# Performance work log

Measured on AMD Instinct MI355X. Metric: run time of the kernel, lower is better.

Reference implementation:

```python
import math
import jax, jax.numpy as jnp
import numpy as np

B, S, HID, NH = 4, 1024, 768, 12
D = HID // NH
R_ACT = 0.5
R_ATTN = 0.5


def act_prune_mask(a, ratio):
    # per-sample kth-smallest magnitude threshold (torch.kthvalue on flatten(1))
    n = int(np.prod(a.shape[1:]))
    k = int(np.clip(n * ratio, 1, n))
    mag = jnp.abs(a)
    thr = jnp.sort(mag.reshape(a.shape[0], -1), axis=1)[:, k - 1]
    thr = thr.reshape((a.shape[0],) + (1,) * (a.ndim - 1))
    return mag >= thr


def setup_inputs() -> dict:
    key = jax.random.key(0)
    ks = jax.random.split(key, 5)
    inp = {
        "hidden_states": jax.random.normal(ks[0], (B, S, HID), dtype=jnp.float32),
        "Wq": jax.random.normal(ks[1], (HID, HID), dtype=jnp.float32) * 0.02,
        "bq": jnp.zeros((HID,), dtype=jnp.float32),
        "Wk": jax.random.normal(ks[2], (HID, HID), dtype=jnp.float32) * 0.02,
        "bk": jnp.zeros((HID,), dtype=jnp.float32),
        "Wv": jax.random.normal(ks[3], (HID, HID), dtype=jnp.float32) * 0.02,
        "bv": jnp.zeros((HID,), dtype=jnp.float32),
        "Wo": jax.random.normal(ks[4], (HID, HID), dtype=jnp.float32) * 0.02,
        "bo": jnp.zeros((HID,), dtype=jnp.float32),
    }
    return inp


def reference(hidden_states, Wq, bq, Wk, bk, Wv, bv, Wo, bo):
    b, s, hid = hidden_states.shape

    # prune mask on input activations (saved for backward in the original; forward math unchanged)
    mask_h = act_prune_mask(hidden_states, R_ACT)
    _hs_prune = jnp.where(mask_h, hidden_states, 0.0)

    q = jnp.matmul(hidden_states, Wq.T) + bq
    k = jnp.matmul(hidden_states, Wk.T) + bk
    v = jnp.matmul(hidden_states, Wv.T) + bv

    def split_heads(x):
        return x.reshape(b, s, NH, D).transpose(0, 2, 1, 3)  # [B,H,S,D]

    q4, k4, v4 = split_heads(q), split_heads(k), split_heads(v)

    mask_q = act_prune_mask(q4, R_ACT)
    mask_k = act_prune_mask(k4, R_ACT)
    _qp = jnp.where(mask_q, q4, 0.0)
    _kp = jnp.where(mask_k, k4, 0.0)

    scores = jnp.einsum("bhqd,bhkd->bhqk", q4, k4) / math.sqrt(D)
    probs = jax.nn.softmax(scores, axis=-1)

    mask_p = act_prune_mask(probs, R_ATTN)
    _pp = jnp.where(mask_p, probs, 0.0)
    mask_v = act_prune_mask(v4, R_ACT)
    _vp = jnp.where(mask_v, v4, 0.0)

    ctx = jnp.einsum("bhqk,bhkd->bhqd", probs, v4)
    ctx = ctx.transpose(0, 2, 1, 3).reshape(b, s, hid)

    mask_c = act_prune_mask(ctx, R_ACT)
    _cp = jnp.where(mask_c, ctx, 0.0)

    out = jnp.matmul(ctx, Wo.T) + bo  # proj_dropout rate = 0.0 (identity)
    return (out, probs)  # vis=True -> weights = attention_probs
```

## Files before the change

### kernel.cpp

```cpp
#include <hip/hip_runtime.h>
#include <hip/hip_bf16.h>

typedef __attribute__((ext_vector_type(4))) float f32x4;
typedef __attribute__((ext_vector_type(8))) short bf16x8;
typedef __attribute__((ext_vector_type(4))) int i32x4;

#define SEQ 1024
#define HIDV 768
#define NH 12
#define HD 64
#define QBLK 64

static __device__ __forceinline__ unsigned short f2b(float f) {
  unsigned u = __builtin_bit_cast(unsigned, f);
  u = (u + 0x7fffu + ((u >> 16) & 1u)) >> 16;
  return (unsigned short)u;
}

static __device__ __forceinline__ void gl16(const unsigned short* g, unsigned short* l) {
  __builtin_amdgcn_global_load_lds(
      (const __attribute__((address_space(1))) unsigned int*)g,
      (__attribute__((address_space(3))) unsigned int*)l, 16, 0, 0);
}

static __device__ __forceinline__ void bar_lgkm() {
  asm volatile("s_waitcnt lgkmcnt(0)" ::: "memory");
  __builtin_amdgcn_sched_barrier(0);
  __builtin_amdgcn_s_barrier();
  __builtin_amdgcn_sched_barrier(0);
}
static __device__ __forceinline__ void bar_only() {
  __builtin_amdgcn_sched_barrier(0);
  __builtin_amdgcn_s_barrier();
  __builtin_amdgcn_sched_barrier(0);
}

__global__ __launch_bounds__(256) void convert_all(
    const float* __restrict__ X, const float* __restrict__ Wq,
    const float* __restrict__ Wk, const float* __restrict__ Wv,
    const float* __restrict__ Wo, unsigned short* __restrict__ dst) {
  long i = (long)blockIdx.x * 256 + threadIdx.x;
  const long N4 = (3145728L + 4 * 589824L) / 4;
  if (i >= N4) return;
  long e = i * 4;
  const float* src; long off;
  if (e < 3145728L)      { src = X;  off = e; }
  else if (e < 3735552L) { src = Wq; off = e - 3145728L; }
  else if (e < 4325376L) { src = Wk; off = e - 3735552L; }
  else if (e < 4915200L) { src = Wv; off = e - 4325376L; }
  else                   { src = Wo; off = e - 4915200L; }
  const float4 v = *reinterpret_cast<const float4*>(src + off);
  ushort4 o;
  o.x = f2b(v.x); o.y = f2b(v.y); o.z = f2b(v.z); o.w = f2b(v.w);
  *reinterpret_cast<ushort4*>(dst + e) = o;
}

__global__ __launch_bounds__(256) void qkv_gemm(
    const unsigned short* __restrict__ Xb,
    const unsigned short* __restrict__ Wqb, const unsigned short* __restrict__ Wkb,
    const unsigned short* __restrict__ Wvb,
    const float* __restrict__ bq, const float* __restrict__ bk, const float* __restrict__ bv,
    unsigned short* __restrict__ Qh, unsigned short* __restrict__ Kh,
    unsigned short* __restrict__ VT) {
  __shared__ __align__(16) unsigned short la[2][128 * 32];
  __shared__ __align__(16) unsigned short lb[2][128 * 32];
  const int z = blockIdx.z;
  const unsigned short* Wb = (z == 0) ? Wqb : (z == 1) ? Wkb : Wvb;
  const float* bias = (z == 0) ? bq : (z == 1) ? bk : bv;
  const int m0 = blockIdx.x * 128, n0 = blockIdx.y * 128;
  const int tid = threadIdx.x;
  const int wave = tid >> 6, lane = tid & 63, g = lane >> 4, c = lane & 15;
  const int wr = (wave >> 1) * 64, wc = (wave & 1) * 64;

  const int sr = wave * 16 + (lane >> 2);
  const int scol = (lane & 3) * 8;
  const unsigned short* Ag = &Xb[(size_t)(m0 + sr) * HIDV + scol];
  const unsigned short* Bg = &Wb[(size_t)(n0 + sr) * HIDV + scol];

  gl16(Ag, &la[0][(wave * 16) * 32]);
  gl16(Ag + (size_t)64 * HIDV, &la[0][(64 + wave * 16) * 32]);
  gl16(Bg, &lb[0][(wave * 16) * 32]);
  gl16(Bg + (size_t)64 * HIDV, &lb[0][(64 + wave * 16) * 32]);
  __syncthreads();

  f32x4 acc[4][4] = {};
  for (int t = 0; t < 24; t++) {
    const int cur = t & 1;
    if (t < 23) {
      const int kt = (t + 1) * 32;
      gl16(Ag + kt, &la[cur ^ 1][(wave * 16) * 32]);
      gl16(Ag + (size_t)64 * HIDV + kt, &la[cur ^ 1][(64 + wave * 16) * 32]);
      gl16(Bg + kt, &lb[cur ^ 1][(wave * 16) * 32]);
      gl16(Bg + (size_t)64 * HIDV + kt, &lb[cur ^ 1][(64 + wave * 16) * 32]);
    }
    bf16x8 af[4], bfr[4];
#pragma unroll
    for (int m = 0; m < 4; m++)
      af[m] = *reinterpret_cast<bf16x8*>(&la[cur][(wr + m * 16 + c) * 32 + g * 8]);
#pragma unroll
    for (int n = 0; n < 4; n++)
      bfr[n] = *reinterpret_cast<bf16x8*>(&lb[cur][(wc + n * 16 + c) * 32 + g * 8]);
#pragma unroll
    for (int m = 0; m < 4; m++)
#pragma unroll
      for (int n = 0; n < 4; n++)
        acc[m][n] = __builtin_amdgcn_mfma_f32_16x16x32_bf16(af[m], bfr[n], acc[m][n], 0, 0, 0);
    __syncthreads();
  }
  float bv4[4];
#pragma unroll
  for (int n = 0; n < 4; n++) bv4[n] = bias[n0 + wc + n * 16 + c];
  if (z < 2) {
    unsigned short* dst = (z == 0) ? Qh : Kh;
#pragma unroll
    for (int m = 0; m < 4; m++) {
      int rb_ = m0 + wr + m * 16 + g * 4;
#pragma unroll
      for (int n = 0; n < 4; n++) {
        int col = n0 + wc + n * 16 + c;
        int h = col >> 6, d = col & 63;
#pragma unroll
        for (int r = 0; r < 4; r++) {
          int row = rb_ + r;
          int b = row >> 10, s = row & 1023;
          dst[((size_t)(b * NH + h) * SEQ + s) * HD + d] = f2b(acc[m][n][r] + bv4[n]);
        }
      }
    }
  } else {
#pragma unroll
    for (int m = 0; m < 4; m++) {
      int rb_ = m0 + wr + m * 16 + g * 4;
      int b = rb_ >> 10, s = rb_ & 1023;
#pragma unroll
      for (int n = 0; n < 4; n++) {
        int col = n0 + wc + n * 16 + c;
        int h = col >> 6, d = col & 63;
        ushort4 o;
        o.x = f2b(acc[m][n][0] + bv4[n]);
        o.y = f2b(acc[m][n][1] + bv4[n]);
        o.z = f2b(acc[m][n][2] + bv4[n]);
        o.w = f2b(acc[m][n][3] + bv4[n]);
        *reinterpret_cast<ushort4*>(&VT[((size_t)(b * NH + h) * HD + d) * SEQ + s]) = o;
      }
    }
  }
}

#define EXPC 0.18033688f
__global__ __launch_bounds__(256) void attn_fused(
    const unsigned short* __restrict__ Qh, const unsigned short* __restrict__ Kh,
    const unsigned short* __restrict__ VT,
    float* __restrict__ probs, unsigned short* __restrict__ CTX) {
  __shared__ __align__(16) unsigned short ldsk[2][64 * 72];
  __shared__ __align__(16) unsigned short ldsv[2][64 * 72];
  __shared__ __align__(16) unsigned short lp[64 * 72];
  const int lin = blockIdx.x;
  const int swz = (lin & 7) * 96 + (lin >> 3);
  const int bh = swz >> 4, rb = (swz & 15) * QBLK;
  const int b = bh / NH, h = bh - b * NH;
  const unsigned short* Qp = Qh + (size_t)bh * SEQ * HD;
  const unsigned short* Kp = Kh + (size_t)bh * SEQ * HD;
  const unsigned short* Vp = VT + (size_t)bh * HD * SEQ;
  float* P = probs + (size_t)bh * SEQ * SEQ;
  const int tid = threadIdx.x, wave = tid >> 6, lane = tid & 63, g = lane >> 4, c = lane & 15;
  const int wrow = wave * 16;
  const int str = tid >> 3;
  const int stc = (tid & 7) * 8;

  bf16x8 aq[2];
#pragma unroll
  for (int ks = 0; ks < 2; ks++)
    aq[ks] = *reinterpret_cast<const bf16x8*>(&Qp[(size_t)(rb + wrow + c) * HD + ks * 32 + g * 8]);

  i32x4 kr0, kr1, vr0, vr1;
  kr0 = *reinterpret_cast<const i32x4*>(&Kp[(size_t)str * HD + stc]);
  kr1 = *reinterpret_cast<const i32x4*>(&Kp[(size_t)(str + 32) * HD + stc]);
  *reinterpret_cast<i32x4*>(&ldsk[0][str * 72 + stc]) = kr0;
  *reinterpret_cast<i32x4*>(&ldsk[0][(str + 32) * 72 + stc]) = kr1;
  bar_lgkm();

  float lsum = 0.f;
  for (int ct = 0; ct < 16; ct++) {
    const int cur = ct & 1;
    if (ct < 15) {
      kr0 = *reinterpret_cast<const i32x4*>(&Kp[(size_t)((ct + 1) * 64 + str) * HD + stc]);
      kr1 = *reinterpret_cast<const i32x4*>(&Kp[(size_t)((ct + 1) * 64 + str + 32) * HD + stc]);
    }
    f32x4 sreg[4] = {};
#pragma unroll
    for (int ks = 0; ks < 2; ks++) {
      bf16x8 kf[4];
#pragma unroll
      for (int kb = 0; kb < 4; kb++)
        kf[kb] = *reinterpret_cast<bf16x8*>(&ldsk[cur][(kb * 16 + c) * 72 + ks * 32 + g * 8]);
#pragma unroll
      for (int kb = 0; kb < 4; kb++)
        sreg[kb] = __builtin_amdgcn_mfma_f32_16x16x32_bf16(kf[kb], aq[ks], sreg[kb], 0, 0, 0);
    }
#pragma unroll
    for (int kb = 0; kb < 4; kb++)
#pragma unroll
      for (int r = 0; r < 4; r++)
        lsum += __builtin_amdgcn_exp2f(sreg[kb][r] * EXPC);
    if (ct < 15) {
      *reinterpret_cast<i32x4*>(&ldsk[cur ^ 1][str * 72 + stc]) = kr0;
      *reinterpret_cast<i32x4*>(&ldsk[cur ^ 1][(str + 32) * 72 + stc]) = kr1;
      bar_lgkm();
    }
  }
  float s = lsum;
  s += __shfl_xor(s, 16);
  s += __shfl_xor(s, 32);
  const float linv = 1.f / s;

  kr0 = *reinterpret_cast<const i32x4*>(&Kp[(size_t)str * HD + stc]);
  kr1 = *reinterpret_cast<const i32x4*>(&Kp[(size_t)(str + 32) * HD + stc]);
  vr0 = *reinterpret_cast<const i32x4*>(&Vp[(size_t)str * SEQ + stc]);
  vr1 = *reinterpret_cast<const i32x4*>(&Vp[(size_t)(str + 32) * SEQ + stc]);
  *reinterpret_cast<i32x4*>(&ldsk[0][str * 72 + stc]) = kr0;
  *reinterpret_cast<i32x4*>(&ldsk[0][(str + 32) * 72 + stc]) = kr1;
  *reinterpret_cast<i32x4*>(&ldsv[0][str * 72 + stc]) = vr0;
  *reinterpret_cast<i32x4*>(&ldsv[0][(str + 32) * 72 + stc]) = vr1;
  bar_lgkm();

  f32x4 acc[4] = {};
  for (int ct = 0; ct < 16; ct++) {
    const int cur = ct & 1;
    if (ct < 15) {
      kr0 = *reinterpret_cast<const i32x4*>(&Kp[(size_t)((ct + 1) * 64 + str) * HD + stc]);
      kr1 = *reinterpret_cast<const i32x4*>(&Kp[(size_t)((ct + 1) * 64 + str + 32) * HD + stc]);
      vr0 = *reinterpret_cast<const i32x4*>(&Vp[(size_t)str * SEQ + (ct + 1) * 64 + stc]);
      vr1 = *reinterpret_cast<const i32x4*>(&Vp[(size_t)(str + 32) * SEQ + (ct + 1) * 64 + stc]);
    }
    f32x4 sreg[4] = {};
#pragma unroll
    for (int ks = 0; ks < 2; ks++) {
      bf16x8 kf[4];
#pragma unroll
      for (int kb = 0; kb < 4; kb++)
        kf[kb] = *reinterpret_cast<bf16x8*>(&ldsk[cur][(kb * 16 + c) * 72 + ks * 32 + g * 8]);
#pragma unroll
      for (int kb = 0; kb < 4; kb++)
        sreg[kb] = __builtin_amdgcn_mfma_f32_16x16x32_bf16(kf[kb], aq[ks], sreg[kb], 0, 0, 0);
    }
    {
      float* Prow = &P[(size_t)(rb + wrow + c) * SEQ + ct * 64];
#pragma unroll
      for (int kb = 0; kb < 4; kb++) {
        f32x4 p;
#pragma unroll
        for (int r = 0; r < 4; r++)
          p[r] = __builtin_amdgcn_exp2f(sreg[kb][r] * EXPC) * linv;
        *reinterpret_cast<f32x4*>(&Prow[kb * 16 + g * 4]) = p;
        uint2 pk;
        pk.x = (unsigned)f2b(p[0]) | ((unsigned)f2b(p[1]) << 16);
        pk.y = (unsigned)f2b(p[2]) | ((unsigned)f2b(p[3]) << 16);
        *reinterpret_cast<uint2*>(&lp[(wrow + c) * 72 + kb * 16 + g * 4]) = pk;
      }
    }
    if (ct < 15) {
      *reinterpret_cast<i32x4*>(&ldsk[cur ^ 1][str * 72 + stc]) = kr0;
      *reinterpret_cast<i32x4*>(&ldsk[cur ^ 1][(str + 32) * 72 + stc]) = kr1;
      *reinterpret_cast<i32x4*>(&ldsv[cur ^ 1][str * 72 + stc]) = vr0;
      *reinterpret_cast<i32x4*>(&ldsv[cur ^ 1][(str + 32) * 72 + stc]) = vr1;
    }
    bar_lgkm();
#pragma unroll
    for (int ks = 0; ks < 2; ks++) {
      bf16x8 pa, vf[4];
      pa = *reinterpret_cast<bf16x8*>(&lp[(wrow + c) * 72 + ks * 32 + g * 8]);
#pragma unroll
      for (int db = 0; db < 4; db++)
        vf[db] = *reinterpret_cast<bf16x8*>(&ldsv[cur][(db * 16 + c) * 72 + ks * 32 + g * 8]);
#pragma unroll
      for (int db = 0; db < 4; db++)
        acc[db] = __builtin_amdgcn_mfma_f32_16x16x32_bf16(pa, vf[db], acc[db], 0, 0, 0);
    }
    bar_only();
  }

#pragma unroll
  for (int db = 0; db < 4; db++)
#pragma unroll
    for (int r = 0; r < 4; r++)
      lp[(wrow + g * 4 + r) * 72 + db * 16 + c] = f2b(acc[db][r]);
  bar_lgkm();
  {
    const int q = tid >> 2, seg = (tid & 3) * 16;
    const unsigned short* src = &lp[q * 72 + seg];
    unsigned short* dst = &CTX[(size_t)(b * SEQ + rb + q) * HIDV + h * HD + seg];
    i32x4 t0 = *reinterpret_cast<const i32x4*>(&src[0]);
    i32x4 t1 = *reinterpret_cast<const i32x4*>(&src[8]);
    *reinterpret_cast<i32x4*>(&dst[0]) = t0;
    *reinterpret_cast<i32x4*>(&dst[8]) = t1;
  }
}

__global__ __launch_bounds__(256) void proj_gemm(
    const unsigned short* __restrict__ Ab, const unsigned short* __restrict__ Wb,
    const float* __restrict__ bias, float* __restrict__ out) {
  __shared__ __align__(16) unsigned short la[2][128 * 32];
  __shared__ __align__(16) unsigned short lb[2][128 * 32];
  const int m0 = blockIdx.x * 128, n0 = blockIdx.y * 128;
  const int tid = threadIdx.x;
  const int wave = tid >> 6, lane = tid & 63, g = lane >> 4, c = lane & 15;
  const int wr = (wave >> 1) * 64, wc = (wave & 1) * 64;
  const int sr = wave * 16 + (lane >> 2);
  const int scol = (lane & 3) * 8;
  const unsigned short* Ag = &Ab[(size_t)(m0 + sr) * HIDV + scol];
  const unsigned short* Bg = &Wb[(size_t)(n0 + sr) * HIDV + scol];

  gl16(Ag, &la[0][(wave * 16) * 32]);
  gl16(Ag + (size_t)64 * HIDV, &la[0][(64 + wave * 16) * 32]);
  gl16(Bg, &lb[0][(wave * 16) * 32]);
  gl16(Bg + (size_t)64 * HIDV, &lb[0][(64 + wave * 16) * 32]);
  __syncthreads();

  f32x4 acc[4][4] = {};
  for (int t = 0; t < 24; t++) {
    const int cur = t & 1;
    if (t < 23) {
      const int kt = (t + 1) * 32;
      gl16(Ag + kt, &la[cur ^ 1][(wave * 16) * 32]);
      gl16(Ag + (size_t)64 * HIDV + kt, &la[cur ^ 1][(64 + wave * 16) * 32]);
      gl16(Bg + kt, &lb[cur ^ 1][(wave * 16) * 32]);
      gl16(Bg + (size_t)64 * HIDV + kt, &lb[cur ^ 1][(64 + wave * 16) * 32]);
    }
    bf16x8 af[4], bfr[4];
#pragma unroll
    for (int m = 0; m < 4; m++)
      af[m] = *reinterpret_cast<bf16x8*>(&la[cur][(wr + m * 16 + c) * 32 + g * 8]);
#pragma unroll
    for (int n = 0; n < 4; n++)
      bfr[n] = *reinterpret_cast<bf16x8*>(&lb[cur][(wc + n * 16 + c) * 32 + g * 8]);
#pragma unroll
    for (int m = 0; m < 4; m++)
#pragma unroll
      for (int n = 0; n < 4; n++)
        acc[m][n] = __builtin_amdgcn_mfma_f32_16x16x32_bf16(af[m], bfr[n], acc[m][n], 0, 0, 0);
    __syncthreads();
  }
  float bv4[4];
#pragma unroll
  for (int n = 0; n < 4; n++) bv4[n] = bias[n0 + wc + n * 16 + c];
#pragma unroll
  for (int m = 0; m < 4; m++) {
    int rb_ = m0 + wr + m * 16 + g * 4;
#pragma unroll
    for (int n = 0; n < 4; n++) {
      int col = n0 + wc + n * 16 + c;
#pragma unroll
      for (int r = 0; r < 4; r++)
        out[(size_t)(rb_ + r) * HIDV + col] = acc[m][n][r] + bv4[n];
    }
  }
}

extern "C" void kernel_launch(void* const* d_in, const int* in_sizes, int n_in,
                              void* d_out, int out_size, void* d_ws, size_t ws_size,
                              hipStream_t stream) {
  const float* X  = (const float*)d_in[0];
  const float* Wq = (const float*)d_in[1];
  const float* bq = (const float*)d_in[2];
  const float* Wk = (const float*)d_in[3];
  const float* bk = (const float*)d_in[4];
  const float* Wv = (const float*)d_in[5];
  const float* bv = (const float*)d_in[6];
  const float* Wo = (const float*)d_in[7];
  const float* bo = (const float*)d_in[8];
  float* out = (float*)d_out;
  float* probs = out + 3145728;

  unsigned short* Xb  = (unsigned short*)d_ws;
  unsigned short* Wqb = Xb + 3145728;
  unsigned short* Wkb = Wqb + 589824;
  unsigned short* Wvb = Wkb + 589824;
  unsigned short* Wob = Wvb + 589824;
  unsigned short* Qh  = Wob + 589824;
  unsigned short* Kh  = Qh + 3145728;
  unsigned short* VT  = Kh + 3145728;
  unsigned short* CTX = VT + 3145728;

  convert_all<<<5376, 256, 0, stream>>>(X, Wq, Wk, Wv, Wo, Xb);
  qkv_gemm<<<dim3(32, 6, 3), 256, 0, stream>>>(Xb, Wqb, Wkb, Wvb, bq, bk, bv, Qh, Kh, VT);
  attn_fused<<<dim3(768), 256, 0, stream>>>(Qh, Kh, VT, probs, CTX);
  proj_gemm<<<dim3(32, 6), 256, 0, stream>>>(CTX, Wob, bo, out);
}
```

Baseline: 113.4 us.

## Triple-buffer GEMM loads, unroll attention loops by two, halve proj tile

The QKV and projection GEMMs move from double to triple-buffered global_load_lds staging with a prefetch distance of two, waiting with partial vmcnt counts instead of full syncthreads. The attention kernel's K/V register prefetch is unrolled by two with separate register sets, so loads for the next-next tile are issued before the current tile's compute. The projection GEMM uses 64-row M tiles to launch twice as many blocks. The aim is to hide global memory latency and raise occupancy, at the cost of more LDS and registers and tricky wait-count correctness.

```diff
diff --git a/kernel.cpp b/kernel.cpp
--- a/kernel.cpp
+++ b/kernel.cpp
@@ -34,6 +34,13 @@
   __builtin_amdgcn_s_barrier();
   __builtin_amdgcn_sched_barrier(0);
 }
+#define BAR_VM(N)                                                         \
+  do {                                                                    \
+    asm volatile("s_waitcnt vmcnt(" #N ") lgkmcnt(0)" ::: "memory");      \
+    __builtin_amdgcn_sched_barrier(0);                                    \
+    __builtin_amdgcn_s_barrier();                                         \
+    __builtin_amdgcn_sched_barrier(0);                                    \
+  } while (0)
 
 __global__ __launch_bounds__(256) void convert_all(
     const float* __restrict__ X, const float* __restrict__ Wq,
@@ -62,8 +69,8 @@
     const float* __restrict__ bq, const float* __restrict__ bk, const float* __restrict__ bv,
     unsigned short* __restrict__ Qh, unsigned short* __restrict__ Kh,
     unsigned short* __restrict__ VT) {
-  __shared__ __align__(16) unsigned short la[2][128 * 32];
-  __shared__ __align__(16) unsigned short lb[2][128 * 32];
+  __shared__ __align__(16) unsigned short la[3][128 * 32];
+  __shared__ __align__(16) unsigned short lb[3][128 * 32];
   const int z = blockIdx.z;
   const unsigned short* Wb = (z == 0) ? Wqb : (z == 1) ? Wkb : Wvb;
   const float* bias = (z == 0) ? bq : (z == 1) ? bk : bv;
@@ -77,22 +84,23 @@
   const unsigned short* Ag = &Xb[(size_t)(m0 + sr) * HIDV + scol];
   const unsigned short* Bg = &Wb[(size_t)(n0 + sr) * HIDV + scol];
 
-  gl16(Ag, &la[0][(wave * 16) * 32]);
-  gl16(Ag + (size_t)64 * HIDV, &la[0][(64 + wave * 16) * 32]);
-  gl16(Bg, &lb[0][(wave * 16) * 32]);
-  gl16(Bg + (size_t)64 * HIDV, &lb[0][(64 + wave * 16) * 32]);
-  __syncthreads();
+#define QKV_STAGE(buf, kt)                                                \
+  do {                                                                    \
+    gl16(Ag + (kt), &la[buf][(wave * 16) * 32]);                          \
+    gl16(Ag + (size_t)64 * HIDV + (kt), &la[buf][(64 + wave * 16) * 32]); \
+    gl16(Bg + (kt), &lb[buf][(wave * 16) * 32]);                          \
+    gl16(Bg + (size_t)64 * HIDV + (kt), &lb[buf][(64 + wave * 16) * 32]); \
+  } while (0)
+
+  QKV_STAGE(0, 0);
+  QKV_STAGE(1, 32);
+  BAR_VM(4);
 
   f32x4 acc[4][4] = {};
+#pragma unroll 3
   for (int t = 0; t < 24; t++) {
-    const int cur = t & 1;
-    if (t < 23) {
-      const int kt = (t + 1) * 32;
-      gl16(Ag + kt, &la[cur ^ 1][(wave * 16) * 32]);
-      gl16(Ag + (size_t)64 * HIDV + kt, &la[cur ^ 1][(64 + wave * 16) * 32]);
-      gl16(Bg + kt, &lb[cur ^ 1][(wave * 16) * 32]);
-      gl16(Bg + (size_t)64 * HIDV + kt, &lb[cur ^ 1][(64 + wave * 16) * 32]);
-    }
+    const int cur = t % 3;
+    if (t < 22) QKV_STAGE((t + 2) % 3, (t + 2) * 32);
     bf16x8 af[4], bfr[4];
 #pragma unroll
     for (int m = 0; m < 4; m++)
@@ -105,8 +113,10 @@
 #pragma unroll
       for (int n = 0; n < 4; n++)
         acc[m][n] = __builtin_amdgcn_mfma_f32_16x16x32_bf16(af[m], bfr[n], acc[m][n], 0, 0, 0);
-    __syncthreads();
-  }
+    if (t < 22)      BAR_VM(4);
+    else if (t < 23) BAR_VM(0);
+  }
+#undef QKV_STAGE
   float bv4[4];
 #pragma unroll
   for (int n = 0; n < 4; n++) bv4[n] = bias[n0 + wc + n * 16 + c];
@@ -173,112 +183,142 @@
   for (int ks = 0; ks < 2; ks++)
     aq[ks] = *reinterpret_cast<const bf16x8*>(&Qp[(size_t)(rb + wrow + c) * HD + ks * 32 + g * 8]);
 
-  i32x4 kr0, kr1, vr0, vr1;
-  kr0 = *reinterpret_cast<const i32x4*>(&Kp[(size_t)str * HD + stc]);
-  kr1 = *reinterpret_cast<const i32x4*>(&Kp[(size_t)(str + 32) * HD + stc]);
-  *reinterpret_cast<i32x4*>(&ldsk[0][str * 72 + stc]) = kr0;
-  *reinterpret_cast<i32x4*>(&ldsk[0][(str + 32) * 72 + stc]) = kr1;
+#define LDK(t, r0, r1)                                                               \
+  do {                                                                               \
+    r0 = *reinterpret_cast<const i32x4*>(&Kp[(size_t)((t)*64 + str) * HD + stc]);    \
+    r1 = *reinterpret_cast<const i32x4*>(&Kp[(size_t)((t)*64 + str + 32) * HD + stc]); \
+  } while (0)
+#define LDV(t, r0, r1)                                                               \
+  do {                                                                               \
+    r0 = *reinterpret_cast<const i32x4*>(&Vp[(size_t)str * SEQ + (t)*64 + stc]);     \
+    r1 = *reinterpret_cast<const i32x4*>(&Vp[(size_t)(str + 32) * SEQ + (t)*64 + stc]); \
+  } while (0)
+#define DSWK(buf, r0, r1)                                              \
+  do {                                                                 \
+    *reinterpret_cast<i32x4*>(&ldsk[buf][str * 72 + stc]) = r0;        \
+    *reinterpret_cast<i32x4*>(&ldsk[buf][(str + 32) * 72 + stc]) = r1; \
+  } while (0)
+#define DSWV(buf, r0, r1)                                              \
+  do {                                                                 \
+    *reinterpret_cast<i32x4*>(&ldsv[buf][str * 72 + stc]) = r0;        \
+    *reinterpret_cast<i32x4*>(&ldsv[buf][(str + 32) * 72 + stc]) = r1; \
+  } while (0)
+#define QKT_TILE(buf, sreg)                                                              \
+  do {                                                                                   \
+    _Pragma("unroll") for (int ks = 0; ks < 2; ks++) {                                   \
+      bf16x8 kf[4];                                                                      \
+      _Pragma("unroll") for (int kb = 0; kb < 4; kb++)                                   \
+          kf[kb] = *reinterpret_cast<bf16x8*>(&ldsk[buf][(kb * 16 + c) * 72 + ks * 32 + g * 8]); \
+      _Pragma("unroll") for (int kb = 0; kb < 4; kb++)                                   \
+          sreg[kb] = __builtin_amdgcn_mfma_f32_16x16x32_bf16(kf[kb], aq[ks], sreg[kb], 0, 0, 0); \
+    }                                                                                    \
+  } while (0)
+
+  i32x4 kA0, kA1, kB0, kB1;
+
+  float lsum = 0.f;
+  LDK(0, kA0, kA1);
+  LDK(1, kB0, kB1);
+  DSWK(0, kA0, kA1);
   bar_lgkm();
-
-  float lsum = 0.f;
-  for (int ct = 0; ct < 16; ct++) {
-    const int cur = ct & 1;
-    if (ct < 15) {
-      kr0 = *reinterpret_cast<const i32x4*>(&Kp[(size_t)((ct + 1) * 64 + str) * HD + stc]);
-      kr1 = *reinterpret_cast<const i32x4*>(&Kp[(size_t)((ct + 1) * 64 + str + 32) * HD + stc]);
-    }
-    f32x4 sreg[4] = {};
-#pragma unroll
-    for (int ks = 0; ks < 2; ks++) {
-      bf16x8 kf[4];
+#pragma unroll 1
+  for (int ct2 = 0; ct2 < 8; ct2++) {
+    const int ct = ct2 * 2;
+    if (ct2 < 7) LDK(ct + 2, kA0, kA1);
+    {
+      f32x4 sreg[4] = {};
+      QKT_TILE(0, sreg);
 #pragma unroll
       for (int kb = 0; kb < 4; kb++)
-        kf[kb] = *reinterpret_cast<bf16x8*>(&ldsk[cur][(kb * 16 + c) * 72 + ks * 32 + g * 8]);
+#pragma unroll
+        for (int r = 0; r < 4; r++) lsum += __builtin_amdgcn_exp2f(sreg[kb][r] * EXPC);
+    }
+    DSWK(1, kB0, kB1);
+    bar_lgkm();
+    if (ct2 < 7) LDK(ct + 3, kB0, kB1);
+    {
+      f32x4 sreg[4] = {};
+      QKT_TILE(1, sreg);
 #pragma unroll
       for (int kb = 0; kb < 4; kb++)
-        sreg[kb] = __builtin_amdgcn_mfma_f32_16x16x32_bf16(kf[kb], aq[ks], sreg[kb], 0, 0, 0);
-    }
-#pragma unroll
-    for (int kb = 0; kb < 4; kb++)
-#pragma unroll
-      for (int r = 0; r < 4; r++)
-        lsum += __builtin_amdgcn_exp2f(sreg[kb][r] * EXPC);
-    if (ct < 15) {
-      *reinterpret_cast<i32x4*>(&ldsk[cur ^ 1][str * 72 + stc]) = kr0;
-      *reinterpret_cast<i32x4*>(&ldsk[cur ^ 1][(str + 32) * 72 + stc]) = kr1;
-      bar_lgkm();
-    }
+#pragma unroll
+        for (int r = 0; r < 4; r++) lsum += __builtin_amdgcn_exp2f(sreg[kb][r] * EXPC);
+    }
+    if (ct2 < 7) DSWK(0, kA0, kA1);
+    bar_lgkm();
   }
   float s = lsum;
   s += __shfl_xor(s, 16);
   s += __shfl_xor(s, 32);
   const float linv = 1.f / s;
 
-  kr0 = *reinterpret_cast<const i32x4*>(&Kp[(size_t)str * HD + stc]);
-  kr1 = *reinterpret_cast<const i32x4*>(&Kp[(size_t)(str + 32) * HD + stc]);
-  vr0 = *reinterpret_cast<const i32x4*>(&Vp[(size_t)str * SEQ + stc]);
-  vr1 = *reinterpret_cast<const i32x4*>(&Vp[(size_t)(str + 32) * SEQ + stc]);
-  *reinterpret_cast<i32x4*>(&ldsk[0][str * 72 + stc]) = kr0;
-  *reinterpret_cast<i32x4*>(&ldsk[0][(str + 32) * 72 + stc]) = kr1;
-  *reinterpret_cast<i32x4*>(&ldsv[0][str * 72 + stc]) = vr0;
-  *reinterpret_cast<i32x4*>(&ldsv[0][(str + 32) * 72 + stc]) = vr1;
+#define PWRITE(ct, sreg)                                                      \
+  do {                                                                        \
+    float* Prow = &P[(size_t)(rb + wrow + c) * SEQ + (ct)*64];                \
+    _Pragma("unroll") for (int kb = 0; kb < 4; kb++) {                        \
+      f32x4 p;                                                                \
+      _Pragma("unroll") for (int r = 0; r < 4; r++)                           \
+          p[r] = __builtin_amdgcn_exp2f(sreg[kb][r] * EXPC) * linv;           \
+      *reinterpret_cast<f32x4*>(&Prow[kb * 16 + g * 4]) = p;                  \
+      uint2 pk;                                                               \
+      pk.x = (unsigned)f2b(p[0]) | ((unsigned)f2b(p[1]) << 16);               \
+      pk.y = (unsigned)f2b(p[2]) | ((unsigned)f2b(p[3]) << 16);               \
+      *reinterpret_cast<uint2*>(&lp[(wrow + c) * 72 + kb * 16 + g * 4]) = pk; \
+    }                                                                         \
+  } while (0)
+#define PV_TILE(buf)                                                                     \
+  do {                                                                                   \
+    _Pragma("unroll") for (int ks = 0; ks < 2; ks++) {                                   \
+      bf16x8 pa, vf[4];                                                                  \
+      pa = *reinterpret_cast<bf16x8*>(&lp[(wrow + c) * 72 + ks * 32 + g * 8]);           \
+      _Pragma("unroll") for (int db = 0; db < 4; db++)                                   \
+          vf[db] = *reinterpret_cast<bf16x8*>(&ldsv[buf][(db * 16 + c) * 72 + ks * 32 + g * 8]); \
+      _Pragma("unroll") for (int db = 0; db < 4; db++)                                   \
+          acc[db] = __builtin_amdgcn_mfma_f32_16x16x32_bf16(pa, vf[db], acc[db], 0, 0, 0); \
+    }                                                                                    \
+  } while (0)
+
+  i32x4 vA0, vA1, vB0, vB1;
+  f32x4 acc[4] = {};
+  LDK(0, kA0, kA1);
+  LDV(0, vA0, vA1);
+  LDK(1, kB0, kB1);
+  LDV(1, vB0, vB1);
+  DSWK(0, kA0, kA1);
+  DSWV(0, vA0, vA1);
   bar_lgkm();
-
-  f32x4 acc[4] = {};
-  for (int ct = 0; ct < 16; ct++) {
-    const int cur = ct & 1;
-    if (ct < 15) {
-      kr0 = *reinterpret_cast<const i32x4*>(&Kp[(size_t)((ct + 1) * 64 + str) * HD + stc]);
-      kr1 = *reinterpret_cast<const i32x4*>(&Kp[(size_t)((ct + 1) * 64 + str + 32) * HD + stc]);
-      vr0 = *reinterpret_cast<const i32x4*>(&Vp[(size_t)str * SEQ + (ct + 1) * 64 + stc]);
-      vr1 = *reinterpret_cast<const i32x4*>(&Vp[(size_t)(str + 32) * SEQ + (ct + 1) * 64 + stc]);
-    }
-    f32x4 sreg[4] = {};
-#pragma unroll
-    for (int ks = 0; ks < 2; ks++) {
-      bf16x8 kf[4];
-#pragma unroll
-      for (int kb = 0; kb < 4; kb++)
-        kf[kb] = *reinterpret_cast<bf16x8*>(&ldsk[cur][(kb * 16 + c) * 72 + ks * 32 + g * 8]);
-#pragma unroll
-      for (int kb = 0; kb < 4; kb++)
-        sreg[kb] = __builtin_amdgcn_mfma_f32_16x16x32_bf16(kf[kb], aq[ks], sreg[kb], 0, 0, 0);
-    }
+#pragma unroll 1
+  for (int ct2 = 0; ct2 < 8; ct2++) {
+    const int ct = ct2 * 2;
+    if (ct2 < 7) { LDK(ct + 2, kA0, kA1); LDV(ct + 2, vA0, vA1); }
     {
-      float* Prow = &P[(size_t)(rb + wrow + c) * SEQ + ct * 64];
-#pragma unroll
-      for (int kb = 0; kb < 4; kb++) {
-        f32x4 p;
-#pragma unroll
-        for (int r = 0; r < 4; r++)
-          p[r] = __builtin_amdgcn_exp2f(sreg[kb][r] * EXPC) * linv;
-        *reinterpret_cast<f32x4*>(&Prow[kb * 16 + g * 4]) = p;
-        uint2 pk;
-        pk.x = (unsigned)f2b(p[0]) | ((unsigned)f2b(p[1]) << 16);
-        pk.y = (unsigned)f2b(p[2]) | ((unsigned)f2b(p[3]) << 16);
-        *reinterpret_cast<uint2*>(&lp[(wrow + c) * 72 + kb * 16 + g * 4]) = pk;
-      }
-    }
-    if (ct < 15) {
-      *reinterpret_cast<i32x4*>(&ldsk[cur ^ 1][str * 72 + stc]) = kr0;
-      *reinterpret_cast<i32x4*>(&ldsk[cur ^ 1][(str + 32) * 72 + stc]) = kr1;
-      *reinterpret_cast<i32x4*>(&ldsv[cur ^ 1][str * 72 + stc]) = vr0;
-      *reinterpret_cast<i32x4*>(&ldsv[cur ^ 1][(str + 32) * 72 + stc]) = vr1;
-    }
+      f32x4 sreg[4] = {};
+      QKT_TILE(0, sreg);
+      PWRITE(ct, sreg);
+    }
+    DSWK(1, kB0, kB1);
+    DSWV(1, vB0, vB1);
     bar_lgkm();
-#pragma unroll
-    for (int ks = 0; ks < 2; ks++) {
-      bf16x8 pa, vf[4];
-      pa = *reinterpret_cast<bf16x8*>(&lp[(wrow + c) * 72 + ks * 32 + g * 8]);
-#pragma unroll
-      for (int db = 0; db < 4; db++)
-        vf[db] = *reinterpret_cast<bf16x8*>(&ldsv[cur][(db * 16 + c) * 72 + ks * 32 + g * 8]);
-#pragma unroll
-      for (int db = 0; db < 4; db++)
-        acc[db] = __builtin_amdgcn_mfma_f32_16x16x32_bf16(pa, vf[db], acc[db], 0, 0, 0);
-    }
+    PV_TILE(0);
     bar_only();
-  }
+    if (ct2 < 7) { LDK(ct + 3, kB0, kB1); LDV(ct + 3, vB0, vB1); }
+    {
+      f32x4 sreg[4] = {};
+      QKT_TILE(1, sreg);
+      PWRITE(ct + 1, sreg);
+    }
+    if (ct2 < 7) { DSWK(0, kA0, kA1); DSWV(0, vA0, vA1); }
+    bar_lgkm();
+    PV_TILE(1);
+    bar_only();
+  }
+#undef LDK
+#undef LDV
+#undef DSWK
+#undef DSWV
+#undef QKT_TILE
+#undef PWRITE
+#undef PV_TILE
 
 #pragma unroll
   for (int db = 0; db < 4; db++)
@@ -300,52 +340,55 @@
 __global__ __launch_bounds__(256) void proj_gemm(
     const unsigned short* __restrict__ Ab, const unsigned short* __restrict__ Wb,
     const float* __restrict__ bias, float* __restrict__ out) {
-  __shared__ __align__(16) unsigned short la[2][128 * 32];
-  __shared__ __align__(16) unsigned short lb[2][128 * 32];
-  const int m0 = blockIdx.x * 128, n0 = blockIdx.y * 128;
+  __shared__ __align__(16) unsigned short la[3][64 * 32];
+  __shared__ __align__(16) unsigned short lb[3][128 * 32];
+  const int m0 = blockIdx.x * 64, n0 = blockIdx.y * 128;
   const int tid = threadIdx.x;
   const int wave = tid >> 6, lane = tid & 63, g = lane >> 4, c = lane & 15;
-  const int wr = (wave >> 1) * 64, wc = (wave & 1) * 64;
-  const int sr = wave * 16 + (lane >> 2);
+  const int wr = (wave >> 1) * 32, wc = (wave & 1) * 64;
+  const int sra = (tid >> 2);
+  const int srb = wave * 16 + (lane >> 2);
   const int scol = (lane & 3) * 8;
-  const unsigned short* Ag = &Ab[(size_t)(m0 + sr) * HIDV + scol];
-  const unsigned short* Bg = &Wb[(size_t)(n0 + sr) * HIDV + scol];
-
-  gl16(Ag, &la[0][(wave * 16) * 32]);
-  gl16(Ag + (size_t)64 * HIDV, &la[0][(64 + wave * 16) * 32]);
-  gl16(Bg, &lb[0][(wave * 16) * 32]);
-  gl16(Bg + (size_t)64 * HIDV, &lb[0][(64 + wave * 16) * 32]);
-  __syncthreads();
-
-  f32x4 acc[4][4] = {};
+  const unsigned short* Ag = &Ab[(size_t)(m0 + sra) * HIDV + scol];
+  const unsigned short* Bg = &Wb[(size_t)(n0 + srb) * HIDV + scol];
+
+#define PROJ_STAGE(buf, kt)                                               \
+  do {                                                                    \
+    gl16(Ag + (kt), &la[buf][(wave * 16) * 32]);                          \
+    gl16(Bg + (kt), &lb[buf][(wave * 16) * 32]);                          \
+    gl16(Bg + (size_t)64 * HIDV + (kt), &lb[buf][(64 + wave * 16) * 32]); \
+  } while (0)
+
+  PROJ_STAGE(0, 0);
+  PROJ_STAGE(1, 32);
+  BAR_VM(3);
+
+  f32x4 acc[2][4] = {};
+#pragma unroll 3
   for (int t = 0; t < 24; t++) {
-    const int cur = t & 1;
-    if (t < 23) {
-      const int kt = (t + 1) * 32;
-      gl16(Ag + kt, &la[cur ^ 1][(wave * 16) * 32]);
-      gl16(Ag + (size_t)64 * HIDV + kt, &la[cur ^ 1][(64 + wave * 16) * 32]);
-      gl16(Bg + kt, &lb[cur ^ 1][(wave * 16) * 32]);
-      gl16(Bg + (size_t)64 * HIDV + kt, &lb[cur ^ 1][(64 + wave * 16) * 32]);
-    }
-    bf16x8 af[4], bfr[4];
-#pragma unroll
-    for (int m = 0; m < 4; m++)
+    const int cur = t % 3;
+    if (t < 22) PROJ_STAGE((t + 2) % 3, (t + 2) * 32);
+    bf16x8 af[2], bfr[4];
+#pragma unroll
+    for (int m = 0; m < 2; m++)
       af[m] = *reinterpret_cast<bf16x8*>(&la[cur][(wr + m * 16 + c) * 32 + g * 8]);
 #pragma unroll
     for (int n = 0; n < 4; n++)
       bfr[n] = *reinterpret_cast<bf16x8*>(&lb[cur][(wc + n * 16 + c) * 32 + g * 8]);
 #pragma unroll
-    for (int m = 0; m < 4; m++)
+    for (int m = 0; m < 2; m++)
 #pragma unroll
       for (int n = 0; n < 4; n++)
         acc[m][n] = __builtin_amdgcn_mfma_f32_16x16x32_bf16(af[m], bfr[n], acc[m][n], 0, 0, 0);
-    __syncthreads();
-  }
+    if (t < 22)      BAR_VM(3);
+    else if (t < 23) BAR_VM(0);
+  }
+#undef PROJ_STAGE
   float bv4[4];
 #pragma unroll
   for (int n = 0; n < 4; n++) bv4[n] = bias[n0 + wc + n * 16 + c];
 #pragma unroll
-  for (int m = 0; m < 4; m++) {
+  for (int m = 0; m < 2; m++) {
     int rb_ = m0 + wr + m * 16 + g * 4;
 #pragma unroll
     for (int n = 0; n < 4; n++) {
@@ -385,5 +428,5 @@
   convert_all<<<5376, 256, 0, stream>>>(X, Wq, Wk, Wv, Wo, Xb);
   qkv_gemm<<<dim3(32, 6, 3), 256, 0, stream>>>(Xb, Wqb, Wkb, Wvb, bq, bk, bv, Qh, Kh, VT);
   attn_fused<<<dim3(768), 256, 0, stream>>>(Qh, Kh, VT, probs, CTX);
-  proj_gemm<<<dim3(32, 6), 256, 0, stream>>>(CTX, Wob, bo, out);
-}
+  proj_gemm<<<dim3(64, 6), 256, 0, stream>>>(CTX, Wob, bo, out);
+}
```

New measurement: 117.3 us. 1.03x slower.
